# Optimization experiments

Measured on AMD Instinct MI355X. Metric: run time of the kernel, lower is better.

## Reference

```python
import jax, jax.numpy as jnp
import numpy as np

N_HEAD = 12
D_HEAD = 64  # key_dim // n_head = 768 // 12


def sparsemax(z):
    # Martins & Astudillo (2016): projection of each row of z onto the simplex.
    K = z.shape[-1]
    z_sorted = -jnp.sort(-z, axis=-1)                      # descending sort
    cs = jnp.cumsum(z_sorted, axis=-1)
    r = jnp.arange(1, K + 1, dtype=z.dtype)
    support = (1.0 + r * z_sorted) > cs                    # support set indicator
    ksz = jnp.sum(support, axis=-1, keepdims=True)         # support size k(z)
    cs_k = jnp.take_along_axis(cs, ksz.astype(jnp.int32) - 1, axis=-1)
    tau = (cs_k - 1.0) / ksz.astype(z.dtype)               # threshold
    return jnp.maximum(z - tau, 0.0)


def setup_inputs() -> dict:
    key = jax.random.key(0)
    kq, kk, kv, kwq, kbq, kwk, kbk = jax.random.split(key, 7)
    B, L, D = 8, 1024, 768
    scale = 0.02
    return {
        "q": jax.random.normal(kq, (B, L, D), jnp.float32),
        "k": jax.random.normal(kk, (B, L, D), jnp.float32),
        "v": jax.random.normal(kv, (B, L, D), jnp.float32),
        "Wq": jax.random.normal(kwq, (D, D), jnp.float32) * scale,  # torch Linear weight [out,in]
        "bq": jax.random.normal(kbq, (D,), jnp.float32) * scale,
        "Wk": jax.random.normal(kwk, (D, D), jnp.float32) * scale,
        "bk": jax.random.normal(kbk, (D,), jnp.float32) * scale,
    }


def reference(q, k, v, Wq, bq, Wk, bk):
    B, Lq, _ = q.shape
    Lkv = k.shape[1]
    # project and split heads: [B, H, L, d_head]
    qh = (q @ Wq.T + bq).reshape(B, Lq, N_HEAD, D_HEAD).transpose(0, 2, 1, 3)
    kh = (k @ Wk.T + bk).reshape(B, Lkv, N_HEAD, D_HEAD).transpose(0, 2, 1, 3)
    inv_sqrt_d = jnp.asarray(1.0 / np.sqrt(D_HEAD), q.dtype)
    scores = jnp.einsum("bhqd,bhkd->bhqk", qh, kh) * inv_sqrt_d  # [B,H,Lq,Lkv]
    attn = sparsemax(scores)
    attn = attn.mean(axis=1)                                      # head-mean -> [B,Lq,Lkv]
    # eval mode: smooth_max is identity (training-only smoothing)
    output = jnp.einsum("bqk,bkd->bqd", attn, v)                  # [B,Lq,Dv]
    return output, attn
```

## Files before the change

### kernel.cpp

```cpp
#include <hip/hip_runtime.h>

#define BSZ 8
#define NH 12
#define LSEQ 1024
#define DMODEL 768
#define DHEAD 64
#define OUT_ELEMS 6291456
#define ATTN_ELEMS 8388608

typedef __attribute__((ext_vector_type(8))) short short8;
typedef __attribute__((ext_vector_type(4))) float f32x4;

__device__ __forceinline__ float wred(float v) {
    v += __shfl_xor(v, 1);
    v += __shfl_xor(v, 2);
    v += __shfl_xor(v, 4);
    v += __shfl_xor(v, 8);
    v += __shfl_xor(v, 16);
    v += __shfl_xor(v, 32);
    return v;
}

__device__ __forceinline__ unsigned short f2bf(float x) {
    union { float f; unsigned u; } c; c.f = x;
    unsigned r = (c.u + 0x7FFF + ((c.u >> 16) & 1)) >> 16;
    return (unsigned short)r;
}
__device__ __forceinline__ float bf2f(unsigned short h) {
    union { float f; unsigned u; } c; c.u = ((unsigned)h) << 16;
    return c.f;
}
__device__ __forceinline__ void split2(float x, unsigned short& h, unsigned short& l) {
    h = f2bf(x);
    l = f2bf(x - bf2f(h));
}

__global__ __launch_bounds__(256) void proj_mfma(
    const float* __restrict__ qin, const float* __restrict__ kin,
    const float* __restrict__ Wq, const float* __restrict__ bq,
    const float* __restrict__ Wk, const float* __restrict__ bk,
    unsigned short* __restrict__ ws) {
    const float* A; const float* W; const float* bias;
    unsigned short* hi; unsigned short* lo;
    if (blockIdx.z == 0) { A = qin; W = Wq; bias = bq; hi = ws;                lo = ws + OUT_ELEMS; }
    else                 { A = kin; W = Wk; bias = bk; hi = ws + 2*OUT_ELEMS; lo = ws + 3*OUT_ELEMS; }

    __shared__ unsigned short Ah[128][32], Al[128][32];
    __shared__ unsigned short Bh[128][32], Bl[128][32];

    const int t    = threadIdx.x;
    const int lane = t & 63;
    const int w    = t >> 6;
    const int wr   = w >> 1, wc = w & 1;
    const int mrow = lane & 15, quad = lane >> 4;
    const int m0   = blockIdx.y * 128;
    const int n0   = blockIdx.x * 128;

    const int srow = t >> 3;
    const int scol = (t & 7) * 4;

    f32x4 acc[4][4];
#pragma unroll
    for (int i = 0; i < 4; ++i)
#pragma unroll
        for (int j = 0; j < 4; ++j) acc[i][j] = (f32x4){0.f, 0.f, 0.f, 0.f};

    for (int k0 = 0; k0 < DMODEL; k0 += 32) {
        float4 av[4], wv[4];
#pragma unroll
        for (int i = 0; i < 4; ++i) {
            av[i] = *(const float4*)&A[(size_t)(m0 + srow + i * 32) * DMODEL + k0 + scol];
            wv[i] = *(const float4*)&W[(size_t)(n0 + srow + i * 32) * DMODEL + k0 + scol];
        }
        __syncthreads();
#pragma unroll
        for (int i = 0; i < 4; ++i) {
            ushort4 h4, l4;
            split2(av[i].x, h4.x, l4.x); split2(av[i].y, h4.y, l4.y);
            split2(av[i].z, h4.z, l4.z); split2(av[i].w, h4.w, l4.w);
            *(ushort4*)&Ah[srow + i * 32][scol] = h4;
            *(ushort4*)&Al[srow + i * 32][scol] = l4;
            split2(wv[i].x, h4.x, l4.x); split2(wv[i].y, h4.y, l4.y);
            split2(wv[i].z, h4.z, l4.z); split2(wv[i].w, h4.w, l4.w);
            *(ushort4*)&Bh[srow + i * 32][scol] = h4;
            *(ushort4*)&Bl[srow + i * 32][scol] = l4;
        }
        __syncthreads();

        short8 ah[4], al[4], bh[4], bl[4];
#pragma unroll
        for (int i = 0; i < 4; ++i) {
            ah[i] = *(const short8*)&Ah[wr * 64 + i * 16 + mrow][quad * 8];
            al[i] = *(const short8*)&Al[wr * 64 + i * 16 + mrow][quad * 8];
            bh[i] = *(const short8*)&Bh[wc * 64 + i * 16 + mrow][quad * 8];
            bl[i] = *(const short8*)&Bl[wc * 64 + i * 16 + mrow][quad * 8];
        }
#pragma unroll
        for (int i = 0; i < 4; ++i)
#pragma unroll
            for (int j = 0; j < 4; ++j) {
                acc[i][j] = __builtin_amdgcn_mfma_f32_16x16x32_bf16(al[i], bh[j], acc[i][j], 0, 0, 0);
                acc[i][j] = __builtin_amdgcn_mfma_f32_16x16x32_bf16(ah[i], bl[j], acc[i][j], 0, 0, 0);
                acc[i][j] = __builtin_amdgcn_mfma_f32_16x16x32_bf16(ah[i], bh[j], acc[i][j], 0, 0, 0);
            }
    }

#pragma unroll
    for (int j = 0; j < 4; ++j) {
        const int ng = n0 + wc * 64 + j * 16 + mrow;
        const float bj = bias[ng];
        const int hh = ng >> 6, dd = ng & 63;
#pragma unroll
        for (int i = 0; i < 4; ++i) {
#pragma unroll
            for (int reg = 0; reg < 4; ++reg) {
                const int mg = m0 + wr * 64 + i * 16 + quad * 4 + reg;
                const float c = acc[i][j][reg] + bj;
                unsigned short ch, cl;
                split2(c, ch, cl);
                const size_t idx = (((size_t)(mg >> 10) * NH + hh) * LSEQ + (mg & 1023)) * DHEAD + dd;
                hi[idx] = ch;
                lo[idx] = cl;
            }
        }
    }
}

__global__ __launch_bounds__(256, 2) void attn_kernel(
    const unsigned short* __restrict__ ws, float* __restrict__ attn_out) {
    __shared__ float S[16 * 1024];

    const unsigned short* Qhi = ws;
    const unsigned short* Qlo = ws + OUT_ELEMS;
    const unsigned short* Khi = ws + 2 * OUT_ELEMS;
    const unsigned short* Klo = ws + 3 * OUT_ELEMS;

    const int t = threadIdx.x;
    const int lane = t & 63;
    const int w = t >> 6;
    const int b = blockIdx.y;
    const int q0 = blockIdx.x * 16;

    const int mrow = lane & 15;
    const int quad = lane >> 4;

    f32x4 acc[16];
#pragma unroll
    for (int j = 0; j < 16; ++j) acc[j] = (f32x4){0.f, 0.f, 0.f, 0.f};

    for (int h = 0; h < NH; ++h) {
        const size_t hb = ((size_t)b * NH + h) * (LSEQ * DHEAD);

        const size_t aoff = hb + (size_t)(q0 + mrow) * DHEAD + quad * 8;
        short8 ah0 = *(const short8*)(Qhi + aoff);
        short8 ah1 = *(const short8*)(Qhi + aoff + 32);
        short8 al0 = *(const short8*)(Qlo + aoff);
        short8 al1 = *(const short8*)(Qlo + aoff + 32);

        __syncthreads();

#pragma unroll 4
        for (int nt = 0; nt < 16; ++nt) {
            const int n0 = w * 256 + nt * 16;
            const size_t boff = hb + (size_t)(n0 + mrow) * DHEAD + quad * 8;
            short8 bh0 = *(const short8*)(Khi + boff);
            short8 bh1 = *(const short8*)(Khi + boff + 32);
            short8 bl0 = *(const short8*)(Klo + boff);
            short8 bl1 = *(const short8*)(Klo + boff + 32);
            f32x4 d = {0.f, 0.f, 0.f, 0.f};
            d = __builtin_amdgcn_mfma_f32_16x16x32_bf16(al0, bh0, d, 0, 0, 0);
            d = __builtin_amdgcn_mfma_f32_16x16x32_bf16(ah0, bl0, d, 0, 0, 0);
            d = __builtin_amdgcn_mfma_f32_16x16x32_bf16(ah0, bh0, d, 0, 0, 0);
            d = __builtin_amdgcn_mfma_f32_16x16x32_bf16(al1, bh1, d, 0, 0, 0);
            d = __builtin_amdgcn_mfma_f32_16x16x32_bf16(ah1, bl1, d, 0, 0, 0);
            d = __builtin_amdgcn_mfma_f32_16x16x32_bf16(ah1, bh1, d, 0, 0, 0);
#pragma unroll
            for (int reg = 0; reg < 4; ++reg)
                S[(quad * 4 + reg) * 1024 + n0 + mrow] = d[reg] * 0.125f;
        }
        __syncthreads();

#pragma unroll
        for (int rr = 0; rr < 4; ++rr) {
            const int r = w * 4 + rr;
            float z[16];
#pragma unroll
            for (int j = 0; j < 16; ++j) z[j] = S[r * 1024 + lane + 64 * j];
            float s0 = 0.f;
#pragma unroll
            for (int j = 0; j < 16; ++j) s0 += z[j];
            float tau = (wred(s0) - 1.0f) * (1.0f / 1024.0f);
            float prev = 1024.0f;
            for (int it = 0; it < 64; ++it) {
                float s = 0.f, c2 = 0.f;
#pragma unroll
                for (int j = 0; j < 16; ++j) {
                    if (z[j] > tau) { s += z[j]; c2 += 1.0f; }
                }
                s = wred(s); c2 = wred(c2);
                if (c2 == prev) break;
                tau = (s - 1.0f) / c2;
                prev = c2;
            }
#pragma unroll
            for (int j = 0; j < 16; ++j) {
                float p = z[j] - tau;
                S[r * 1024 + lane + 64 * j] = p > 0.f ? p : 0.f;
            }
        }
        __syncthreads();

#pragma unroll
        for (int j = 0; j < 16; ++j) {
            f32x4 vv = *(const f32x4*)&S[j * 1024 + t * 4];
            acc[j] += vv;
        }
    }

    float* ao = attn_out + ((size_t)b * LSEQ + q0) * LSEQ;
#pragma unroll
    for (int j = 0; j < 16; ++j) {
        f32x4 o = acc[j] * (1.0f / 12.0f);
        *(f32x4*)&ao[(size_t)j * LSEQ + t * 4] = o;
    }
}

__global__ __launch_bounds__(256) void out_mfma(
    const float* __restrict__ attn, const float* __restrict__ v,
    float* __restrict__ out) {
    const int b = blockIdx.z;
    const float* Ab = attn + (size_t)b * LSEQ * LSEQ;
    const float* Vb = v    + (size_t)b * LSEQ * DMODEL;
    float* Cb       = out  + (size_t)b * LSEQ * DMODEL;

    __shared__ unsigned short Ah[128][32], Al[128][32];
    __shared__ unsigned short Bh[128][36], Bl[128][36];

    const int t    = threadIdx.x;
    const int lane = t & 63;
    const int w    = t >> 6;
    const int wr   = w >> 1, wc = w & 1;
    const int mrow = lane & 15, quad = lane >> 4;
    const int m0   = blockIdx.y * 128;
    const int n0   = blockIdx.x * 128;

    const int srow = t >> 3;
    const int scol = (t & 7) * 4;
    const int bn   = t & 127;
    const int bk0  = (t >> 7) * 16;

    f32x4 acc[4][4];
#pragma unroll
    for (int i = 0; i < 4; ++i)
#pragma unroll
        for (int j = 0; j < 4; ++j) acc[i][j] = (f32x4){0.f, 0.f, 0.f, 0.f};

    for (int k0 = 0; k0 < LSEQ; k0 += 32) {
        float4 av[4];
#pragma unroll
        for (int i = 0; i < 4; ++i)
            av[i] = *(const float4*)&Ab[(size_t)(m0 + srow + i * 32) * LSEQ + k0 + scol];
        float bv[16];
#pragma unroll
        for (int i = 0; i < 16; ++i)
            bv[i] = Vb[(size_t)(k0 + bk0 + i) * DMODEL + n0 + bn];

        __syncthreads();
#pragma unroll
        for (int i = 0; i < 4; ++i) {
            ushort4 h4, l4;
            split2(av[i].x, h4.x, l4.x); split2(av[i].y, h4.y, l4.y);
            split2(av[i].z, h4.z, l4.z); split2(av[i].w, h4.w, l4.w);
            *(ushort4*)&Ah[srow + i * 32][scol] = h4;
            *(ushort4*)&Al[srow + i * 32][scol] = l4;
        }
#pragma unroll
        for (int g = 0; g < 4; ++g) {
            ushort4 h4, l4;
            split2(bv[g * 4 + 0], h4.x, l4.x); split2(bv[g * 4 + 1], h4.y, l4.y);
            split2(bv[g * 4 + 2], h4.z, l4.z); split2(bv[g * 4 + 3], h4.w, l4.w);
            *(ushort4*)&Bh[bn][bk0 + g * 4] = h4;
            *(ushort4*)&Bl[bn][bk0 + g * 4] = l4;
        }
        __syncthreads();

        short8 ah[4], al[4], bh[4], bl[4];
#pragma unroll
        for (int i = 0; i < 4; ++i) {
            ah[i] = *(const short8*)&Ah[wr * 64 + i * 16 + mrow][quad * 8];
            al[i] = *(const short8*)&Al[wr * 64 + i * 16 + mrow][quad * 8];
        }
#pragma unroll
        for (int j = 0; j < 4; ++j) {
            const unsigned short* ph = &Bh[wc * 64 + j * 16 + mrow][quad * 8];
            const unsigned short* pl = &Bl[wc * 64 + j * 16 + mrow][quad * 8];
            uint2 h0 = *(const uint2*)ph;
            uint2 h1 = *(const uint2*)(ph + 4);
            uint2 l0 = *(const uint2*)pl;
            uint2 l1 = *(const uint2*)(pl + 4);
            union { uint u[4]; short8 s; } ch, cl;
            ch.u[0] = h0.x; ch.u[1] = h0.y; ch.u[2] = h1.x; ch.u[3] = h1.y;
            cl.u[0] = l0.x; cl.u[1] = l0.y; cl.u[2] = l1.x; cl.u[3] = l1.y;
            bh[j] = ch.s; bl[j] = cl.s;
        }
#pragma unroll
        for (int i = 0; i < 4; ++i)
#pragma unroll
            for (int j = 0; j < 4; ++j) {
                acc[i][j] = __builtin_amdgcn_mfma_f32_16x16x32_bf16(al[i], bh[j], acc[i][j], 0, 0, 0);
                acc[i][j] = __builtin_amdgcn_mfma_f32_16x16x32_bf16(ah[i], bl[j], acc[i][j], 0, 0, 0);
                acc[i][j] = __builtin_amdgcn_mfma_f32_16x16x32_bf16(ah[i], bh[j], acc[i][j], 0, 0, 0);
            }
    }

#pragma unroll
    for (int i = 0; i < 4; ++i)
#pragma unroll
        for (int j = 0; j < 4; ++j)
#pragma unroll
            for (int reg = 0; reg < 4; ++reg) {
                const int mg = m0 + wr * 64 + i * 16 + quad * 4 + reg;
                const int ng = n0 + wc * 64 + j * 16 + mrow;
                Cb[(size_t)mg * DMODEL + ng] = acc[i][j][reg];
            }
}

extern "C" void kernel_launch(void* const* d_in, const int* in_sizes, int n_in,
                              void* d_out, int out_size, void* d_ws, size_t ws_size,
                              hipStream_t stream) {
    const float* q  = (const float*)d_in[0];
    const float* k  = (const float*)d_in[1];
    const float* v  = (const float*)d_in[2];
    const float* Wq = (const float*)d_in[3];
    const float* bq = (const float*)d_in[4];
    const float* Wk = (const float*)d_in[5];
    const float* bk = (const float*)d_in[6];

    float* out  = (float*)d_out;
    float* attn = out + OUT_ELEMS;
    unsigned short* ws = (unsigned short*)d_ws;

    hipLaunchKernelGGL(proj_mfma, dim3(6, 64, 2), dim3(256), 0, stream,
                       q, k, Wq, bq, Wk, bk, ws);
    hipLaunchKernelGGL(attn_kernel, dim3(64, 8), dim3(256), 0, stream,
                       ws, attn);
    hipLaunchKernelGGL(out_mfma, dim3(6, 8, 8), dim3(256), 0, stream,
                       attn, v, out);
}
```

Measured before the change: 600.3 us.

## Batch sparsemax threshold iteration across four rows with DPP reductions and ballot counts

Reworks the per-row sparsemax threshold search so each wave processes its four rows together. Wave reductions use DPP row operations plus a readlane instead of shfl_xor, and support counts come from ballot/popcount. The initial tau is raised to max(mean-based, max-1), which should cut the number of fixed-point iterations. Shared memory reads and writes become vectorised float4. The cost is more registers (64 floats of z per thread), which may lower occupancy, and all four rows now run until the slowest one converges.

```diff
diff --git a/kernel.cpp b/kernel.cpp
--- a/kernel.cpp
+++ b/kernel.cpp
@@ -11,15 +11,8 @@
 typedef __attribute__((ext_vector_type(8))) short short8;
 typedef __attribute__((ext_vector_type(4))) float f32x4;
 
-__device__ __forceinline__ float wred(float v) {
-    v += __shfl_xor(v, 1);
-    v += __shfl_xor(v, 2);
-    v += __shfl_xor(v, 4);
-    v += __shfl_xor(v, 8);
-    v += __shfl_xor(v, 16);
-    v += __shfl_xor(v, 32);
-    return v;
-}
+__device__ __forceinline__ int   f2i(float x) { union { float f; int i; } c; c.f = x; return c.i; }
+__device__ __forceinline__ float i2f(int x)   { union { int i; float f; } c; c.i = x; return c.f; }
 
 __device__ __forceinline__ unsigned short f2bf(float x) {
     union { float f; unsigned u; } c; c.f = x;
@@ -33,6 +26,34 @@
 __device__ __forceinline__ void split2(float x, unsigned short& h, unsigned short& l) {
     h = f2bf(x);
     l = f2bf(x - bf2f(h));
+}
+
+template<int CTRL>
+__device__ __forceinline__ float dppadd(float v) {
+    return v + i2f(__builtin_amdgcn_update_dpp(0, f2i(v), CTRL, 0xF, 0xF, true));
+}
+template<int CTRL>
+__device__ __forceinline__ float dppmax(float v) {
+    return fmaxf(v, i2f(__builtin_amdgcn_update_dpp(f2i(v), f2i(v), CTRL, 0xF, 0xF, false)));
+}
+
+__device__ __forceinline__ void wsum4(float s[4]) {
+#define WS(CTRL) _Pragma("unroll") for (int rr = 0; rr < 4; ++rr) { s[rr] = dppadd<CTRL>(s[rr]); }
+    WS(0x111) WS(0x112) WS(0x114) WS(0x118) WS(0x142) WS(0x143)
+#undef WS
+#pragma unroll
+    for (int rr = 0; rr < 4; ++rr) s[rr] = i2f(__builtin_amdgcn_readlane(f2i(s[rr]), 63));
+}
+
+__device__ __forceinline__ void wsummax4(float s[4], float m[4]) {
+#define WS(CTRL) _Pragma("unroll") for (int rr = 0; rr < 4; ++rr) { s[rr] = dppadd<CTRL>(s[rr]); m[rr] = dppmax<CTRL>(m[rr]); }
+    WS(0x111) WS(0x112) WS(0x114) WS(0x118) WS(0x142) WS(0x143)
+#undef WS
+#pragma unroll
+    for (int rr = 0; rr < 4; ++rr) {
+        s[rr] = i2f(__builtin_amdgcn_readlane(f2i(s[rr]), 63));
+        m[rr] = i2f(__builtin_amdgcn_readlane(f2i(m[rr]), 63));
+    }
 }
 
 __global__ __launch_bounds__(256) void proj_mfma(
@@ -180,32 +201,68 @@
         }
         __syncthreads();
 
-#pragma unroll
-        for (int rr = 0; rr < 4; ++rr) {
-            const int r = w * 4 + rr;
-            float z[16];
-#pragma unroll
-            for (int j = 0; j < 16; ++j) z[j] = S[r * 1024 + lane + 64 * j];
-            float s0 = 0.f;
-#pragma unroll
-            for (int j = 0; j < 16; ++j) s0 += z[j];
-            float tau = (wred(s0) - 1.0f) * (1.0f / 1024.0f);
-            float prev = 1024.0f;
+        {
+            float z[4][16];
+            float sv[4], mv[4];
+#pragma unroll
+            for (int rr = 0; rr < 4; ++rr) {
+                const int r = w * 4 + rr;
+#pragma unroll
+                for (int c = 0; c < 4; ++c)
+                    *(f32x4*)&z[rr][c * 4] = *(const f32x4*)&S[r * 1024 + c * 256 + lane * 4];
+                float s = 0.f, m = z[rr][0];
+#pragma unroll
+                for (int j = 0; j < 16; ++j) s += z[rr][j];
+#pragma unroll
+                for (int j = 1; j < 16; ++j) m = fmaxf(m, z[rr][j]);
+                sv[rr] = s; mv[rr] = m;
+            }
+            wsummax4(sv, mv);
+
+            float tau[4]; int prev[4]; bool done[4];
+#pragma unroll
+            for (int rr = 0; rr < 4; ++rr) {
+                tau[rr] = fmaxf((sv[rr] - 1.0f) * (1.0f / 1024.0f), mv[rr] - 1.0f);
+                prev[rr] = -1; done[rr] = false;
+            }
+
             for (int it = 0; it < 64; ++it) {
-                float s = 0.f, c2 = 0.f;
-#pragma unroll
-                for (int j = 0; j < 16; ++j) {
-                    if (z[j] > tau) { s += z[j]; c2 += 1.0f; }
+                float s4[4]; int c4[4];
+#pragma unroll
+                for (int rr = 0; rr < 4; ++rr) {
+                    float s = 0.f; int c = 0;
+#pragma unroll
+                    for (int j = 0; j < 16; ++j) {
+                        bool gt = z[rr][j] > tau[rr];
+                        c += __popcll(__ballot(gt));
+                        s += gt ? z[rr][j] : 0.f;
+                    }
+                    s4[rr] = s; c4[rr] = c;
                 }
-                s = wred(s); c2 = wred(c2);
-                if (c2 == prev) break;
-                tau = (s - 1.0f) / c2;
-                prev = c2;
-            }
-#pragma unroll
-            for (int j = 0; j < 16; ++j) {
-                float p = z[j] - tau;
-                S[r * 1024 + lane + 64 * j] = p > 0.f ? p : 0.f;
+                wsum4(s4);
+                bool alldone = true;
+#pragma unroll
+                for (int rr = 0; rr < 4; ++rr) {
+                    if (!done[rr]) {
+                        if (c4[rr] == prev[rr]) done[rr] = true;
+                        else { tau[rr] = (s4[rr] - 1.0f) / (float)c4[rr]; prev[rr] = c4[rr]; }
+                    }
+                    alldone = alldone && done[rr];
+                }
+                if (alldone) break;
+            }
+
+#pragma unroll
+            for (int rr = 0; rr < 4; ++rr) {
+                const int r = w * 4 + rr;
+#pragma unroll
+                for (int c = 0; c < 4; ++c) {
+                    f32x4 p;
+#pragma unroll
+                    for (int j = 0; j < 4; ++j)
+                        p[j] = fmaxf(z[rr][c * 4 + j] - tau[rr], 0.f);
+                    *(f32x4*)&S[r * 1024 + c * 256 + lane * 4] = p;
+                }
             }
         }
         __syncthreads();
```

New measurement: 554.0 us. 7.7% less time.
